# Performance work log

Measured on AMD Instinct MI355X. Metric: run time of the kernel, lower is better.

## Reference

```python
import jax, jax.numpy as jnp
import numpy as np

IN_DIM, OUT_DIM = 256, 10
N_EXPERTS, N_MEM, STEPS, N_SUB, MAX_K = 12, 32, 6, 5, 5
EXPERT_DIMS = [2048, 2560, 3072, 3584, 4096, 2304, 2816, 3328, 3840, 4608, 3072, 4096]
MAX_E = 4608
N_ITEMS = 4096
SCALE = IN_DIM ** -0.5

def _gelu(x):
    return jax.nn.gelu(x, approximate=False)

_ACTS = [jax.nn.silu, _gelu, lambda x: x * jnp.tanh(jax.nn.softplus(x)), jax.nn.relu,
         jax.nn.selu, jnp.tanh, jax.nn.softplus, jax.nn.elu]
EXPERT_ACTS = [_ACTS[i % 8] for i in range(N_EXPERTS)]

def _ln(x, s, b, eps=1e-5):
    mu = jnp.mean(x, -1, keepdims=True)
    var = jnp.mean((x - mu) ** 2, -1, keepdims=True)
    return (x - mu) * jax.lax.rsqrt(var + eps) * s + b

def _cell(x, ln_s, ln_b, w1, b1, w2, b2):
    h = _gelu(_ln(x, ln_s, ln_b) @ w1.T + b1)
    return x + h @ w2.T + b2

def _ctx_attn(cur, bank, qw, kw, vw):
    q = cur @ qw.T
    k = bank @ kw.T
    v = bank @ vw.T
    attn = jax.nn.softmax(jnp.einsum('nd,ntd->nt', q, k) * SCALE, axis=-1)
    return jnp.einsum('nt,ntd->nd', attn, v)

def _renorm_sparse_topk(probs, active_k):
    tv, ti = jax.lax.top_k(probs, MAX_K)
    mask = (jnp.arange(MAX_K)[None, :] < active_k[:, None]).astype(probs.dtype)
    vals = tv * mask
    rows = jnp.arange(probs.shape[0])[:, None]
    sparse = jnp.zeros_like(probs).at[rows, ti].set(vals)
    return sparse / jnp.maximum(jnp.sum(sparse, -1, keepdims=True), 1e-6)

def _fwd(x, W, b,
         shared_up_w, shared_down_w, shared_ln_s, shared_ln_b, shared_scale,
         mem_keys, mem_vals, mem_q_w, mem_out_w, mem_wg_w, mem_wg_b, mem_wv_w, mem_wv_b,
         depth_q_w, depth_k_w, depth_v_w, depth_out_w,
         rc_ln_s, rc_ln_b, rc_w1, rc_b1, rc_w2, rc_b2,
         ssm_in_w, ssm_out_w, ssm_decay,
         sub_w, sub_b, gate_w, gate_b,
         budget_w, budget_b,
         exp_up, exp_down, exp_ln_s, exp_ln_b,
         halt_w, halt_b,
         aux_up_w, aux_down_w, aux_ln_s, aux_ln_b, aux_gate_w, aux_gate_b,
         rf_ln_s, rf_ln_b, rf_w1, rf_b1, rf_w2, rf_b2, reflect_out_w,
         coll_q_w, coll_k_w, coll_v_w, coll_out_w,
         revisit_w, revisit_b,
         vc_ln_s, vc_ln_b, vc_w1, vc_b1, vc_w2, vc_b2,
         ver_q_w, ver_k_w, ver_v_w, ver_out_w, ver_gate_w, ver_gate_b, correction_out_w,
         mix):
    n = x.shape[0]
    base = x @ W.T + b
    shared = _ln(jax.nn.silu(x @ shared_up_w.T) @ shared_down_w.T, shared_ln_s, shared_ln_b)
    aux = _ln(_gelu(x @ aux_up_w.T) @ aux_down_w.T, aux_ln_s, aux_ln_b)

    mem_vals_b = jnp.broadcast_to(mem_vals[None], (n, N_MEM, IN_DIM))
    current = x
    mem_logits = jnp.zeros_like(base)
    depth_logits = jnp.zeros_like(base)
    cum_halt = jnp.zeros((n, 1), x.dtype)
    bank = []
    for s in range(STEPS):
        q = current @ mem_q_w.T
        attn = jax.nn.softmax((q @ mem_keys.T) * SCALE, axis=-1)
        mem_read = jnp.einsum('ns,nsd->nd', attn, mem_vals_b)
        wg = jax.nn.sigmoid(jnp.concatenate([current, mem_read], -1) @ mem_wg_w.T + mem_wg_b)
        wv = current @ mem_wv_w.T + mem_wv_b
        mem_vals_b = mem_vals_b * (1.0 - wg[..., None]) + wg[..., None] * wv[:, None, :]
        if bank:
            depth_ctx = _ctx_attn(current, jnp.stack(bank, 1), depth_q_w, depth_k_w, depth_v_w)
        else:
            depth_ctx = jnp.zeros_like(current)
        current = _cell(current + mem_read + depth_ctx,
                        rc_ln_s[s], rc_ln_b[s], rc_w1[s], rc_b1[s], rc_w2[s], rc_b2[s])
        h = jnp.tanh(current @ ssm_in_w.T) * jax.nn.sigmoid(ssm_decay)
        current = current + h @ ssm_out_w.T
        bank.append(current)
        halt = jax.nn.sigmoid((current @ halt_w[s])[:, None] + halt_b[s])
        w_step = (1.0 - cum_halt) * halt
        mem_logits = mem_logits + w_step * (mem_read @ mem_out_w.T)
        depth_logits = depth_logits + w_step * (depth_ctx @ depth_out_w.T)
        cum_halt = jnp.minimum(cum_halt + halt, 1.0)

    sub_logits = jnp.einsum('nd,sed->nse', current, sub_w) + sub_b
    sub_probs = jax.nn.softmax(sub_logits, axis=-1)
    gate = jax.nn.softmax(current @ gate_w.T + gate_b, axis=-1)
    probs = jnp.einsum('ns,nse->ne', gate, sub_probs)
    active_k = jnp.argmax(current @ budget_w.T + budget_b, axis=-1) + 1
    sparse = _renorm_sparse_topk(probs, active_k)

    expert_out = jnp.zeros_like(base)
    for i in range(N_EXPERTS):
        h = EXPERT_ACTS[i](current @ exp_up[i].T)
        o = _ln(h @ exp_down[i].T, exp_ln_s[i], exp_ln_b[i])
        expert_out = expert_out + sparse[:, i:i + 1] * o

    r = current
    for i in range(3):
        r = _cell(r, rf_ln_s[i], rf_ln_b[i], rf_w1[i], rf_b1[i], rf_w2[i], rf_b2[i])
    reflect_logits = r @ reflect_out_w.T

    stack = jnp.stack(bank, 1)
    coll_ctx = _ctx_attn(current, stack, coll_q_w, coll_k_w, coll_v_w)
    coll_logits = coll_ctx @ coll_out_w.T
    revisit = jax.nn.sigmoid(jnp.concatenate([x, current, coll_ctx], -1) @ revisit_w.T + revisit_b)

    v = current
    for i in range(2):
        v = _cell(v, vc_ln_s[i], vc_ln_b[i], vc_w1[i], vc_b1[i], vc_w2[i], vc_b2[i])
    ver_ctx = _ctx_attn(v, stack, ver_q_w, ver_k_w, ver_v_w)
    vg = jax.nn.softmax(jnp.concatenate([v, ver_ctx], -1) @ ver_gate_w.T + ver_gate_b, axis=-1)
    ver_logits = ver_ctx @ ver_out_w.T
    corr_logits = v @ correction_out_w.T

    ag = jax.nn.softmax(x @ aux_gate_w.T + aux_gate_b, axis=-1)
    alpha, beta, gamma, delta, eps_, zeta = [jnp.tanh(mix[i]) for i in range(6)]
    logits = (base
              + shared_scale * (ag[:, :1] * shared + ag[:, 1:] * aux)
              + alpha * expert_out
              + beta * mem_logits + zeta * depth_logits
              + gamma * reflect_logits
              + delta * revisit * coll_logits
              + eps_ * (vg[:, :1] * ver_logits + vg[:, 1:] * corr_logits))
    return logits


def setup_inputs() -> dict:
    key = jax.random.key(0)
    ks = iter(jax.random.split(key, 128))
    def nrm(shape, std=0.02):
        return jax.random.normal(next(ks), shape, jnp.float32) * std
    d, o = IN_DIM, OUT_DIM
    inp = dict(
        x=jax.random.normal(next(ks), (N_ITEMS, d), jnp.float32),
        W=nrm((o, d), 0.05), b=jnp.zeros((o,), jnp.float32),
        shared_up_w=nrm((3072, d)), shared_down_w=nrm((o, 3072)),
        shared_ln_s=jnp.ones((o,)), shared_ln_b=jnp.zeros((o,)),
        shared_scale=jnp.float32(1.0),
        mem_keys=nrm((N_MEM, d)), mem_vals=nrm((N_MEM, d)),
        mem_q_w=nrm((d, d), 0.01), mem_out_w=nrm((o, d), 0.01),
        mem_wg_w=nrm((N_MEM, 2 * d), 0.01), mem_wg_b=jnp.zeros((N_MEM,)),
        mem_wv_w=nrm((d, d), 0.01), mem_wv_b=jnp.zeros((d,)),
        depth_q_w=nrm((d, d), 0.01), depth_k_w=nrm((d, d), 0.01),
        depth_v_w=nrm((d, d), 0.01), depth_out_w=nrm((o, d), 0.01),
        rc_ln_s=jnp.ones((STEPS, d)), rc_ln_b=jnp.zeros((STEPS, d)),
        rc_w1=nrm((STEPS, 896, d)), rc_b1=jnp.zeros((STEPS, 896)),
        rc_w2=nrm((STEPS, d, 896)), rc_b2=jnp.zeros((STEPS, d)),
        ssm_in_w=nrm((48, d)), ssm_out_w=nrm((d, 48)), ssm_decay=jnp.zeros((48,)),
        sub_w=nrm((N_SUB, N_EXPERTS, d)), sub_b=jnp.zeros((N_SUB, N_EXPERTS)),
        gate_w=nrm((N_SUB, d)), gate_b=jnp.zeros((N_SUB,)),
        budget_w=nrm((MAX_K, d), 0.01), budget_b=jnp.zeros((MAX_K,)),
        halt_w=nrm((STEPS, d), 0.01), halt_b=jnp.full((STEPS,), -2.0, jnp.float32),
        aux_up_w=nrm((4096, d)), aux_down_w=nrm((o, 4096)),
        aux_ln_s=jnp.ones((o,)), aux_ln_b=jnp.zeros((o,)),
        aux_gate_w=nrm((2, d), 0.01), aux_gate_b=jnp.zeros((2,)),
        rf_ln_s=jnp.ones((3, d)), rf_ln_b=jnp.zeros((3, d)),
        rf_w1=nrm((3, 1280, d)), rf_b1=jnp.zeros((3, 1280)),
        rf_w2=nrm((3, d, 1280)), rf_b2=jnp.zeros((3, d)),
        reflect_out_w=nrm((o, d), 0.01),
        coll_q_w=nrm((d, d), 0.01), coll_k_w=nrm((d, d), 0.01),
        coll_v_w=nrm((d, d), 0.01), coll_out_w=nrm((o, d), 0.01),
        revisit_w=nrm((1, 3 * d), 0.01), revisit_b=jnp.zeros((1,)),
        vc_ln_s=jnp.ones((2, d)), vc_ln_b=jnp.zeros((2, d)),
        vc_w1=nrm((2, 1536, d)), vc_b1=jnp.zeros((2, 1536)),
        vc_w2=nrm((2, d, 1536)), vc_b2=jnp.zeros((2, d)),
        ver_q_w=nrm((d, d), 0.01), ver_k_w=nrm((d, d), 0.01),
        ver_v_w=nrm((d, d), 0.01), ver_out_w=nrm((o, d), 0.01),
        ver_gate_w=nrm((2, 2 * d), 0.01), ver_gate_b=jnp.zeros((2,)),
        correction_out_w=nrm((o, d), 0.01),
        mix=jnp.full((6,), 0.5, jnp.float32),
    )
    up = jax.random.normal(next(ks), (N_EXPERTS, MAX_E, d), jnp.float32) * 0.02
    down = jax.random.normal(next(ks), (N_EXPERTS, o, MAX_E), jnp.float32) * 0.01
    col = jnp.arange(MAX_E)
    dims = jnp.array(EXPERT_DIMS)
    mask = (col[None, :] < dims[:, None]).astype(jnp.float32)
    inp['exp_up'] = up * mask[:, :, None]
    inp['exp_down'] = down * mask[:, None, :]
    inp['exp_ln_s'] = jnp.ones((N_EXPERTS, o))
    inp['exp_ln_b'] = jnp.zeros((N_EXPERTS, o))
    return inp


def reference(x, W, b,
              shared_up_w, shared_down_w, shared_ln_s, shared_ln_b, shared_scale,
              mem_keys, mem_vals, mem_q_w, mem_out_w, mem_wg_w, mem_wg_b, mem_wv_w, mem_wv_b,
              depth_q_w, depth_k_w, depth_v_w, depth_out_w,
              rc_ln_s, rc_ln_b, rc_w1, rc_b1, rc_w2, rc_b2,
              ssm_in_w, ssm_out_w, ssm_decay,
              sub_w, sub_b, gate_w, gate_b,
              budget_w, budget_b,
              exp_up, exp_down, exp_ln_s, exp_ln_b,
              halt_w, halt_b,
              aux_up_w, aux_down_w, aux_ln_s, aux_ln_b, aux_gate_w, aux_gate_b,
              rf_ln_s, rf_ln_b, rf_w1, rf_b1, rf_w2, rf_b2, reflect_out_w,
              coll_q_w, coll_k_w, coll_v_w, coll_out_w,
              revisit_w, revisit_b,
              vc_ln_s, vc_ln_b, vc_w1, vc_b1, vc_w2, vc_b2,
              ver_q_w, ver_k_w, ver_v_w, ver_out_w, ver_gate_w, ver_gate_b, correction_out_w,
              mix):
    return _fwd(x, W, b,
                shared_up_w, shared_down_w, shared_ln_s, shared_ln_b, shared_scale,
                mem_keys, mem_vals, mem_q_w, mem_out_w, mem_wg_w, mem_wg_b, mem_wv_w, mem_wv_b,
                depth_q_w, depth_k_w, depth_v_w, depth_out_w,
                rc_ln_s, rc_ln_b, rc_w1, rc_b1, rc_w2, rc_b2,
                ssm_in_w, ssm_out_w, ssm_decay,
                sub_w, sub_b, gate_w, gate_b,
                budget_w, budget_b,
                exp_up, exp_down, exp_ln_s, exp_ln_b,
                halt_w, halt_b,
                aux_up_w, aux_down_w, aux_ln_s, aux_ln_b, aux_gate_w, aux_gate_b,
                rf_ln_s, rf_ln_b, rf_w1, rf_b1, rf_w2, rf_b2, reflect_out_w,
                coll_q_w, coll_k_w, coll_v_w, coll_out_w,
                revisit_w, revisit_b,
                vc_ln_s, vc_ln_b, vc_w1, vc_b1, vc_w2, vc_b2,
                ver_q_w, ver_k_w, ver_v_w, ver_out_w, ver_gate_w, ver_gate_b, correction_out_w,
                mix)
```

## Files before the change

### kernel.cpp

```cpp
#include <hip/hip_runtime.h>


constexpr int NI      = 4096;
constexpr int DIM     = 256;
constexpr int ODIM    = 10;
constexpr int NMEM_   = 32;
constexpr int NSTEPS_ = 6;
constexpr int NEXPERT_= 12;
constexpr int MAXE    = 4608;
constexpr int TOTCOL  = 46592;
#define SCL 0.0625f

__constant__ int GCNT[14]   = {8,10,12,14,16,9,11,13,15,18,12,16,12,16};
__constant__ int GSTART[14] = {0,8,18,30,44,60,69,80,93,108,126,138,154,166};
__constant__ int CCNT[14]   = {32,40,48,56,64,36,44,52,60,72,48,64,48,64};
__constant__ int ZCOL[14]   = {0,2048,4608,7680,11264,15360,17664,20480,
                               23808,27648,32256,35328,39424,42496};

typedef __attribute__((ext_vector_type(8))) short short8v;
typedef __attribute__((ext_vector_type(4))) float float4v;
typedef __attribute__((ext_vector_type(4))) unsigned short ushort4v;


__device__ __forceinline__ float wred_sum(float v){
  #pragma unroll
  for (int m = 32; m > 0; m >>= 1) v += __shfl_xor(v, m, 64);
  return v;
}
__device__ __forceinline__ float wred_max(float v){
  #pragma unroll
  for (int m = 32; m > 0; m >>= 1) v = fmaxf(v, __shfl_xor(v, m, 64));
  return v;
}
__device__ __forceinline__ float sigm(float x){ return 1.f/(1.f + __expf(-x)); }
__device__ __forceinline__ float tanh_f(float x){
  float e = __expf(2.f*fabsf(x));
  float r = 1.f - 2.f/(e + 1.f);
  return copysignf(r, x);
}
__device__ __forceinline__ float erf_f(float x){
  float ax = fabsf(x);
  float t = 1.f/fmaf(0.3275911f, ax, 1.f);
  float p = t*(0.254829592f + t*(-0.284496736f + t*(1.421413741f +
            t*(-1.453152027f + t*1.061405429f))));
  float r = 1.f - p*__expf(-ax*ax);
  return copysignf(r, x);
}
__device__ __forceinline__ float geluf(float x){
  return 0.5f*x*(1.f + erf_f(x*0.70710678118654752f));
}
__device__ __forceinline__ float softplusf(float x){
  return fmaxf(x, 0.f) + __logf(1.f + __expf(-fabsf(x)));
}
__device__ __forceinline__ float act_apply(int a, float x){
  switch(a){
    case 0: return x*sigm(x);
    case 1: return geluf(x);
    case 2: return x*tanh_f(softplusf(x));
    case 3: return fmaxf(x, 0.f);
    case 4: { const float l=1.0507009873554805f, al=1.6732632423543772f;
              return x > 0.f ? l*x : l*al*(__expf(x)-1.f); }
    case 5: return tanh_f(x);
    case 6: return softplusf(x);
    default: return x > 0.f ? x : __expf(x)-1.f;
  }
}
__device__ __forceinline__ unsigned short f2b(float f){
  unsigned u = __float_as_uint(f);
  u = u + 0x7FFFu + ((u >> 16) & 1u);
  return (unsigned short)(u >> 16);
}
__device__ __forceinline__ float b2f(unsigned short u){
  return __uint_as_float((unsigned)u << 16);
}
__device__ __forceinline__ float dot256f(const float* __restrict__ a,
                                         const float* __restrict__ w, float s){
  for (int k = 0; k < DIM; k += 4){
    float4 av = *(const float4*)&a[k];
    float4 wv = *(const float4*)&w[k];
    s = fmaf(av.x,wv.x, fmaf(av.y,wv.y, fmaf(av.z,wv.z, fmaf(av.w,wv.w, s))));
  }
  return s;
}
__device__ __forceinline__ void ln10(const float* p, const float* s, const float* b, float* o){
  float mu = 0.f;
  #pragma unroll
  for (int i=0;i<ODIM;i++) mu += p[i];
  mu *= 0.1f;
  float var = 0.f;
  #pragma unroll
  for (int i=0;i<ODIM;i++){ float d = p[i]-mu; var += d*d; }
  var *= 0.1f;
  float rs = 1.f/sqrtf(var + 1e-5f);
  #pragma unroll
  for (int i=0;i<ODIM;i++) o[i] = (p[i]-mu)*rs*s[i] + b[i];
}

__global__ __launch_bounds__(256)
void cvt_k(const float* __restrict__ in, unsigned short* __restrict__ out, int n)
{
  int idx = (blockIdx.x*256 + threadIdx.x)*4;
  if (idx + 3 < n){
    float4 v = *(const float4*)&in[idx];
    ushort4v t; t[0]=f2b(v.x); t[1]=f2b(v.y); t[2]=f2b(v.z); t[3]=f2b(v.w);
    *(ushort4v*)&out[idx] = t;
  }
}

__global__ __launch_bounds__(512)
void cvtup_k(const float* __restrict__ exp_up, const float* __restrict__ shared_up,
             const float* __restrict__ aux_up, short* __restrict__ upb)
{
  int chunk = blockIdx.x;
  int z = 0, crem = chunk;
  while (crem >= CCNT[z]){ crem -= CCNT[z]; z++; }
  const float* src;
  if (z < 12)       src = exp_up + (size_t)z*MAXE*DIM;
  else if (z == 12) src = shared_up;
  else              src = aux_up;
  int colbase = crem*64;
  short* dst = upb + (size_t)chunk*16384;
  int t = threadIdx.x;
  int c = t >> 3, kb = (t & 7)*32;
  const float* srow = src + (size_t)(colbase + c)*DIM + kb;
  #pragma unroll
  for (int j = 0; j < 4; j++){
    float4 f0 = *(const float4*)&srow[j*8];
    float4 f1 = *(const float4*)&srow[j*8+4];
    short8v s;
    s[0]=(short)f2b(f0.x); s[1]=(short)f2b(f0.y); s[2]=(short)f2b(f0.z); s[3]=(short)f2b(f0.w);
    s[4]=(short)f2b(f1.x); s[5]=(short)f2b(f1.y); s[6]=(short)f2b(f1.z); s[7]=(short)f2b(f1.w);
    int kq = (t & 7)*4 + j;
    *(short8v*)&dst[((size_t)kq*64 + c)*8] = s;
  }
}

template<int EPI>
__global__ __launch_bounds__(256)
void gemm_k(const float* __restrict__ A, const float* __restrict__ W,
            const float* __restrict__ bias, const float* __restrict__ R,
            float* __restrict__ C, float* __restrict__ C2, int N, int K)
{
  __shared__ float As[32][68];
  __shared__ float Ws[32][68];
  const int bm = blockIdx.y*64, bn = blockIdx.x*64;
  const int tid = threadIdx.x;
  const int tx = tid & 15, ty = tid >> 4;
  const int lrow = tid >> 2, lkq = (tid & 3) * 8;
  float acc[4][4] = {};
  for (int k0 = 0; k0 < K; k0 += 32){
    #pragma unroll
    for (int h = 0; h < 2; ++h){
      int kk = lkq + h*4;
      float4 va = *(const float4*)&A[(size_t)(bm+lrow)*K + k0 + kk];
      float4 vw = *(const float4*)&W[(size_t)(bn+lrow)*K + k0 + kk];
      As[kk+0][lrow]=va.x; As[kk+1][lrow]=va.y; As[kk+2][lrow]=va.z; As[kk+3][lrow]=va.w;
      Ws[kk+0][lrow]=vw.x; Ws[kk+1][lrow]=vw.y; Ws[kk+2][lrow]=vw.z; Ws[kk+3][lrow]=vw.w;
    }
    __syncthreads();
    #pragma unroll
    for (int kk = 0; kk < 32; ++kk){
      float4 a4 = *(const float4*)&As[kk][ty*4];
      float4 b4 = *(const float4*)&Ws[kk][tx*4];
      float av[4] = {a4.x,a4.y,a4.z,a4.w};
      float bv[4] = {b4.x,b4.y,b4.z,b4.w};
      #pragma unroll
      for (int i=0;i<4;i++)
        #pragma unroll
        for (int j=0;j<4;j++) acc[i][j] = fmaf(av[i], bv[j], acc[i][j]);
    }
    __syncthreads();
  }
  #pragma unroll
  for (int i=0;i<4;i++){
    int r = bm + ty*4 + i;
    #pragma unroll
    for (int j=0;j<4;j++){
      int c = bn + tx*4 + j;
      float v = acc[i][j];
      if constexpr (EPI==0){ C[(size_t)r*N + c] = v; }
      else if constexpr (EPI==1){ C[(size_t)r*N + c] = v + bias[c]; }
      else if constexpr (EPI==2){ C[(size_t)r*N + c] = geluf(v + bias[c]); }
      else if constexpr (EPI==3){ C[(size_t)r*N + c] = v + bias[c] + R[(size_t)r*N + c]; }
      else if constexpr (EPI==6){
        if (c < 256) C[(size_t)r*256 + c] = v + bias[c];
        else C2[(size_t)r*256 + (c-256)] = v;
      }
    }
  }
}

__global__ __launch_bounds__(256)
void gemm_rc1_k(const float* __restrict__ A, const float* __restrict__ W,
                const float* __restrict__ bias, float* __restrict__ C,
                int N, int K)
{
  __shared__ float As[32][132];
  __shared__ float Ws[32][68];
  const int bm = blockIdx.y*128, bn = blockIdx.x*64;
  const int tid = threadIdx.x;
  const int tx = tid & 15, ty = tid >> 4;
  const int arow = tid >> 1, ak = (tid & 1)*16;
  const int brow = tid >> 2, bk = (tid & 3)*8;
  float acc[8][4] = {};
  for (int k0 = 0; k0 < K; k0 += 32){
    float4 a0 = *(const float4*)&A[(size_t)(bm+arow)*K + k0 + ak];
    float4 a1 = *(const float4*)&A[(size_t)(bm+arow)*K + k0 + ak + 4];
    float4 a2 = *(const float4*)&A[(size_t)(bm+arow)*K + k0 + ak + 8];
    float4 a3 = *(const float4*)&A[(size_t)(bm+arow)*K + k0 + ak + 12];
    float4 b0 = *(const float4*)&W[(size_t)(bn+brow)*K + k0 + bk];
    float4 b1 = *(const float4*)&W[(size_t)(bn+brow)*K + k0 + bk + 4];
    As[ak+ 0][arow]=a0.x; As[ak+ 1][arow]=a0.y; As[ak+ 2][arow]=a0.z; As[ak+ 3][arow]=a0.w;
    As[ak+ 4][arow]=a1.x; As[ak+ 5][arow]=a1.y; As[ak+ 6][arow]=a1.z; As[ak+ 7][arow]=a1.w;
    As[ak+ 8][arow]=a2.x; As[ak+ 9][arow]=a2.y; As[ak+10][arow]=a2.z; As[ak+11][arow]=a2.w;
    As[ak+12][arow]=a3.x; As[ak+13][arow]=a3.y; As[ak+14][arow]=a3.z; As[ak+15][arow]=a3.w;
    Ws[bk+0][brow]=b0.x; Ws[bk+1][brow]=b0.y; Ws[bk+2][brow]=b0.z; Ws[bk+3][brow]=b0.w;
    Ws[bk+4][brow]=b1.x; Ws[bk+5][brow]=b1.y; Ws[bk+6][brow]=b1.z; Ws[bk+7][brow]=b1.w;
    __syncthreads();
    #pragma unroll
    for (int kk = 0; kk < 32; ++kk){
      float a8[8];
      *(float4*)&a8[0] = *(const float4*)&As[kk][ty*8];
      *(float4*)&a8[4] = *(const float4*)&As[kk][ty*8+4];
      float4 b4 = *(const float4*)&Ws[kk][tx*4];
      float bv[4] = {b4.x,b4.y,b4.z,b4.w};
      #pragma unroll
      for (int i=0;i<8;i++)
        #pragma unroll
        for (int j=0;j<4;j++) acc[i][j] = fmaf(a8[i], bv[j], acc[i][j]);
    }
    __syncthreads();
  }
  #pragma unroll
  for (int i=0;i<8;i++){
    int r = bm + ty*8 + i;
    #pragma unroll
    for (int j=0;j<4;j++){
      int c = bn + tx*4 + j;
      C[(size_t)r*N + c] = geluf(acc[i][j] + bias[c]);
    }
  }
}

template<int EPI>
__global__ __launch_bounds__(256)
void bgemm_k(const short* __restrict__ A, const short* __restrict__ B,
             const float* __restrict__ bias, const float* __restrict__ R,
             float* __restrict__ Cf, unsigned short* __restrict__ Cb,
             int N, int K)
{
  __shared__ short As[128][40];
  __shared__ short Bsm[64][40];
  const int bm = blockIdx.y*128, bn = blockIdx.x*64;
  const int tid = threadIdx.x;
  const int wave = tid >> 6, lane = tid & 63;
  const int l15 = lane & 15, lg = lane >> 4;
  const int ar = tid >> 1, ah = tid & 1;
  float4v acc[2][4] = {};
  for (int k0 = 0; k0 < K; k0 += 32){
    __syncthreads();
    { const short* src = A + (size_t)(bm+ar)*K + k0 + ah*16;
      short8v v0 = *(const short8v*)src;
      short8v v1 = *(const short8v*)(src+8);
      *(short8v*)&As[ar][ah*16]   = v0;
      *(short8v*)&As[ar][ah*16+8] = v1; }
    if (tid < 128){
      const short* src = B + (size_t)(bn+ar)*K + k0 + ah*16;
      short8v v0 = *(const short8v*)src;
      short8v v1 = *(const short8v*)(src+8);
      *(short8v*)&Bsm[ar][ah*16]   = v0;
      *(short8v*)&Bsm[ar][ah*16+8] = v1; }
    __syncthreads();
    short8v bfr[4];
    #pragma unroll
    for (int nt = 0; nt < 4; nt++)
      bfr[nt] = *(const short8v*)&Bsm[nt*16 + l15][lg*8];
    #pragma unroll
    for (int mt = 0; mt < 2; mt++){
      short8v a = *(const short8v*)&As[wave*32 + mt*16 + l15][lg*8];
      #pragma unroll
      for (int nt = 0; nt < 4; nt++)
        acc[mt][nt] = __builtin_amdgcn_mfma_f32_16x16x32_bf16(a, bfr[nt], acc[mt][nt], 0, 0, 0);
    }
  }
  #pragma unroll
  for (int mt = 0; mt < 2; mt++)
    #pragma unroll
    for (int nt = 0; nt < 4; nt++)
      #pragma unroll
      for (int reg = 0; reg < 4; reg++){
        int row = bm + wave*32 + mt*16 + lg*4 + reg;
        int col = bn + nt*16 + l15;
        float v = acc[mt][nt][reg];
        if constexpr (EPI==0){
          v = geluf(v + bias[col]);
          Cb[(size_t)row*N + col] = f2b(v);
        } else {
          v = v + bias[col] + R[(size_t)row*N + col];
          Cf[(size_t)row*N + col] = v;
        }
      }
}

template<int ACT>
__global__ __launch_bounds__(512)
void moe6_k(const unsigned short* __restrict__ curb, const unsigned short* __restrict__ xb,
            const short* __restrict__ upb,
            const float* __restrict__ exp_down, const float* __restrict__ shared_down,
            const float* __restrict__ aux_down,
            const int* __restrict__ idxl, const int* __restrict__ cnt,
            unsigned short* __restrict__ part,
            int z0, int z1, int z2)
{
  __shared__ short Bs[16384];
  __shared__ float Ds[64][12];
  int gy = blockIdx.y;
  int z = z0;
  if (z1 >= 0 && gy >= GCNT[z]){
    gy -= GCNT[z]; z = z1;
    if (z2 >= 0 && gy >= GCNT[z]){ gy -= GCNT[z]; z = z2; }
  }
  const int n = (z < 12) ? cnt[z] : NI;
  const int bm = blockIdx.x*128;
  if (bm >= n) return;
  const int g = GSTART[z] + gy;
  const int localcol = gy*256;
  int dstride; const float* down;
  if (z < 12){ down = exp_down + (size_t)z*ODIM*MAXE; dstride = MAXE; }
  else if (z == 12){ down = shared_down; dstride = 3072; }
  else { down = aux_down; dstride = 4096; }
  const unsigned short* X = (z < 12) ? curb : xb;
  const int tid = threadIdx.x, wave = tid >> 6, lane = tid & 63;
  const int l15 = lane & 15, lg = lane >> 4;

  int slotA = bm + wave*16 + l15;
  int itemA;
  if (z < 12) itemA = idxl[(size_t)z*NI + ((slotA < n) ? slotA : (n-1))];
  else        itemA = slotA;

  short8v afrag[8];
  { const unsigned short* xr = X + (size_t)itemA*DIM;
    #pragma unroll
    for (int ks = 0; ks < 8; ks++)
      afrag[ks] = *(const short8v*)&xr[ks*32 + lg*8];
  }
  float racc[4][10];
  #pragma unroll
  for (int r = 0; r < 4; r++)
    #pragma unroll
    for (int o = 0; o < 10; o++) racc[r][o] = 0.f;

  const int gchunk0 = (ZCOL[z] + localcol) >> 6;
  const int dso = tid >> 6, dse = tid & 63;

  short8v p0, p1, p2, p3;
  float e0, e1;
  auto ldchunk = [&](int ch){
    const short* chunk = upb + ((size_t)(gchunk0 + ch))*16384;
    p0 = *(const short8v*)&chunk[(size_t)(tid       )*8];
    p1 = *(const short8v*)&chunk[(size_t)(tid +  512)*8];
    p2 = *(const short8v*)&chunk[(size_t)(tid + 1024)*8];
    p3 = *(const short8v*)&chunk[(size_t)(tid + 1536)*8];
    int cb = localcol + ch*64;
    e0 = down[(size_t)dso*dstride + cb + dse];
    e1 = (tid < 128) ? down[(size_t)(dso+8)*dstride + cb + dse] : 0.f;
  };
  auto stu = [&](int u, short8v v){
    int c = u & 63, kq = u >> 6;
    int byteoff = ((c << 9) + (kq << 4)) ^ ((c & 7) << 4);
    *(short8v*)((char*)Bs + byteoff) = v;
  };

  ldchunk(0);
  for (int ch = 0; ch < 4; ++ch){
    stu(tid, p0); stu(tid + 512, p1); stu(tid + 1024, p2); stu(tid + 1536, p3);
    Ds[dse][dso] = e0;
    if (tid < 128) Ds[dse][dso + 8] = e1;
    __syncthreads();
    if (ch < 3) ldchunk(ch + 1);
    float4v acc[4] = {};
    #pragma unroll
    for (int ks = 0; ks < 8; ks++)
      #pragma unroll
      for (int nt = 0; nt < 4; nt++){
        int c = nt*16 + l15, kq = ks*4 + lg;
        int byteoff = ((c << 9) + (kq << 4)) ^ ((c & 7) << 4);
        short8v b = *(const short8v*)((const char*)Bs + byteoff);
        acc[nt] = __builtin_amdgcn_mfma_f32_16x16x32_bf16(afrag[ks], b, acc[nt], 0, 0, 0);
      }
    #pragma unroll
    for (int nt = 0; nt < 4; nt++){
      const float* dp = &Ds[nt*16 + l15][0];
      float4 dv0 = *(const float4*)dp;
      float4 dv1 = *(const float4*)(dp + 4);
      float  d8 = dp[8], d9 = dp[9];
      float dv[10] = {dv0.x,dv0.y,dv0.z,dv0.w,dv1.x,dv1.y,dv1.z,dv1.w,d8,d9};
      float hv[4];
      #pragma unroll
      for (int reg = 0; reg < 4; reg++) hv[reg] = act_apply(ACT, acc[nt][reg]);
      #pragma unroll
      for (int o = 0; o < 10; o++)
        #pragma unroll
        for (int reg = 0; reg < 4; reg++)
          racc[reg][o] = fmaf(hv[reg], dv[o], racc[reg][o]);
    }
    __syncthreads();
  }
  #pragma unroll
  for (int reg = 0; reg < 4; reg++)
    #pragma unroll
    for (int o = 0; o < 10; o++){
      float v = racc[reg][o];
      v += __shfl_xor(v, 1, 64); v += __shfl_xor(v, 2, 64);
      v += __shfl_xor(v, 4, 64); v += __shfl_xor(v, 8, 64);
      racc[reg][o] = v;
    }
  if (l15 == 0){
    #pragma unroll
    for (int reg = 0; reg < 4; reg++){
      int slotW = bm + wave*16 + lg*4 + reg;
      int itemW;
      if (z < 12) itemW = idxl[(size_t)z*NI + ((slotW < n) ? slotW : (n-1))];
      else        itemW = slotW;
      #pragma unroll
      for (int o = 0; o < 10; o++)
        part[((size_t)g*NI + itemW)*ODIM + o] = f2b(racc[reg][o]);
    }
  }
}

__global__ __launch_bounds__(256)
void red_k(const unsigned short* __restrict__ part, float* __restrict__ expert_pre,
           float* __restrict__ shared_pre, float* __restrict__ aux_pre)
{
  int idx = blockIdx.x*256 + threadIdx.x;
  if (idx >= 14*NI*ODIM) return;
  int z = idx / (NI*ODIM), rem = idx - z*NI*ODIM;
  float s = 0.f;
  int g0 = GSTART[z], gn = GCNT[z];
  for (int g2 = 0; g2 < gn; g2++)
    s += b2f(part[(size_t)(g0 + g2)*NI*ODIM + rem]);
  if (z < 12) expert_pre[(size_t)z*NI*ODIM + rem] = s;
  else if (z == 12) shared_pre[rem] = s;
  else aux_pre[rem] = s;
}

__global__ void atb_k(const float* __restrict__ A, const float* __restrict__ B,
                      float* __restrict__ C, int M, int I, int J)
{
  int idx = blockIdx.x*256 + threadIdx.x;
  if (idx >= I*J) return;
  int i = idx / J, j = idx - i*J;
  float s = 0.f;
  for (int m = 0; m < M; m++) s = fmaf(A[(size_t)m*I+i], B[(size_t)m*J+j], s);
  C[idx] = s;
}
__global__ void ab_k(const float* __restrict__ A, const float* __restrict__ B,
                     float* __restrict__ C, int M, int K, int N)
{
  int idx = blockIdx.x*256 + threadIdx.x;
  if (idx >= M*N) return;
  int i = idx / N, j = idx - i*N;
  float s = 0.f;
  for (int k = 0; k < K; k++) s = fmaf(A[(size_t)i*K+k], B[(size_t)k*N+j], s);
  C[idx] = s;
}

__global__ __launch_bounds__(256)
void ln3_k(const float* __restrict__ a, const float* __restrict__ b,
           const float* __restrict__ c, const float* __restrict__ lns,
           const float* __restrict__ lnb, float* __restrict__ xout,
           float* __restrict__ lnout, unsigned short* __restrict__ lnout_b)
{
  int item = blockIdx.x*4 + (threadIdx.x >> 6);
  int lane = threadIdx.x & 63;
  float4 v = ((const float4*)(a + (size_t)item*DIM))[lane];
  if (b){ float4 t = ((const float4*)(b + (size_t)item*DIM))[lane]; v.x+=t.x; v.y+=t.y; v.z+=t.z; v.w+=t.w; }
  if (c){ float4 t = ((const float4*)(c + (size_t)item*DIM))[lane]; v.x+=t.x; v.y+=t.y; v.z+=t.z; v.w+=t.w; }
  if (xout) ((float4*)(xout + (size_t)item*DIM))[lane] = v;
  float mu = wred_sum(v.x+v.y+v.z+v.w) * (1.f/DIM);
  float dx=v.x-mu, dy=v.y-mu, dz=v.z-mu, dw=v.w-mu;
  float var = wred_sum(dx*dx+dy*dy+dz*dz+dw*dw) * (1.f/DIM);
  float rs = 1.f/sqrtf(var + 1e-5f);
  float4 s4 = ((const float4*)lns)[lane];
  float4 b4 = ((const float4*)lnb)[lane];
  float4 o4 = make_float4(dx*rs*s4.x + b4.x, dy*rs*s4.y + b4.y,
                          dz*rs*s4.z + b4.z, dw*rs*s4.w + b4.w);
  if (lnout) ((float4*)(lnout + (size_t)item*DIM))[lane] = o4;
  if (lnout_b){
    ushort4v t; t[0]=f2b(o4.x); t[1]=f2b(o4.y); t[2]=f2b(o4.z); t[3]=f2b(o4.w);
    *(ushort4v*)(lnout_b + (size_t)item*DIM + lane*4) = t;
  }
}

__global__ __launch_bounds__(256)
void memrw_k(const float* __restrict__ cur, const float* __restrict__ MK,
             const float* __restrict__ mem_vals, const float* __restrict__ wv_hist,
             const float* __restrict__ mem_wg_w, const float* __restrict__ mem_wg_b,
             float* __restrict__ a_state, float* __restrict__ c_state,
             float* __restrict__ mem_read, int step)
{
  __shared__ float smem[4][DIM];
  int wi = threadIdx.x >> 6;
  int item = blockIdx.x*4 + wi;
  int lane = threadIdx.x & 63;
  float v = -1e30f;
  if (lane < NMEM_)
    v = dot256f(cur + (size_t)item*DIM, MK + (size_t)lane*DIM, 0.f) * SCL;
  float m = wred_max(v);
// ... 422 lines not shown
  const float* vc_b1         = (const float*)d_in[59];
  const float* vc_w2         = (const float*)d_in[60];
  const float* vc_b2         = (const float*)d_in[61];
  const float* ver_q_w       = (const float*)d_in[62];
  const float* ver_k_w       = (const float*)d_in[63];
  const float* ver_v_w       = (const float*)d_in[64];
  const float* ver_out_w     = (const float*)d_in[65];
  const float* ver_gate_w    = (const float*)d_in[66];
  const float* ver_gate_b    = (const float*)d_in[67];
  const float* correction_out_w = (const float*)d_in[68];
  const float* mix           = (const float*)d_in[69];
  const float* exp_up        = (const float*)d_in[70];
  const float* exp_down      = (const float*)d_in[71];
  const float* exp_ln_s      = (const float*)d_in[72];
  const float* exp_ln_b      = (const float*)d_in[73];
  float* out = (float*)d_out;

  float* w = (float*)d_ws;
  size_t off = 0;
  auto WS = [&](size_t nf){ float* p = w + off; off += nf; return p; };
  float* bank      = WS((size_t)NSTEPS_*NI*DIM);
  float* rbuf      = WS((size_t)NI*DIM);
  float* vbuf      = WS((size_t)NI*DIM);
  float* coll_ctx  = WS((size_t)NI*DIM);
  float* ver_ctx   = WS((size_t)NI*DIM);
  float* q2        = WS((size_t)NI*DIM);
  float* wsumb     = WS((size_t)NI*DIM);
  float* sparse    = WS((size_t)NI*NEXPERT_);
  float* base10    = WS((size_t)NI*ODIM);
  float* reflect10 = WS((size_t)NI*ODIM);
  float* coll10    = WS((size_t)NI*ODIM);
  float* ver10     = WS((size_t)NI*ODIM);
  float* corr10    = WS((size_t)NI*ODIM);
  float* PcT       = WS((size_t)DIM*DIM);
  float* PvT       = WS((size_t)DIM*DIM);
  float* MK        = WS((size_t)NMEM_*DIM);
  float* Wvq       = WS((size_t)512*DIM);
  float* expert_pre= WS((size_t)NEXPERT_*NI*ODIM);
  float* shared_pre= WS((size_t)NI*ODIM);
  float* aux_pre   = WS((size_t)NI*ODIM);
  unsigned short* cur_b = (unsigned short*)WS((size_t)NI*DIM/2);
  unsigned short* x_b   = (unsigned short*)WS((size_t)NI*DIM/2);
  int* idxl        = (int*)WS((size_t)NEXPERT_*NI);
  float* S72       = WS((size_t)NI*72);
  int* cnt         = (int*)WS(16);
  float* zbase     = w + off;
  float* mem_logits   = WS((size_t)NI*ODIM);
  float* depth_logits = WS((size_t)NI*ODIM);
  float* cum_halt     = WS((size_t)NI);
  size_t zbytes = (size_t)((w + off) - zbase) * sizeof(float);
  hipMemsetAsync((void*)zbase, 0, zbytes, stream);

  float* U = w + off;
  float* wv_hist   = U;
  float* hbig      = U + (size_t)NSTEPS_*NI*DIM;
  float* cur_in    = hbig + (size_t)NI*896;
  float* t_ln      = cur_in + (size_t)NI*DIM;
  float* mem_read  = t_ln + (size_t)NI*DIM;
  float* depth_ctx = mem_read + (size_t)NI*DIM;
  float* a_state   = depth_ctx + (size_t)NI*DIM;
  float* c_state   = a_state + (size_t)NI*NMEM_;
  unsigned short* upb    = (unsigned short*)U;
  unsigned short* hb     = (unsigned short*)U;
  float* ovl = U + 5963776;
  unsigned short* t_ln_b = (unsigned short*)ovl;          ovl += 524288;
  unsigned short* rfw1b  = (unsigned short*)ovl;          ovl += 491520;
  unsigned short* rfw2b  = (unsigned short*)ovl;          ovl += 491520;
  unsigned short* vcw1b  = (unsigned short*)ovl;          ovl += 393216;
  unsigned short* vcw2b  = (unsigned short*)ovl;          ovl += 393216;
  unsigned short* part   = (unsigned short*)ovl;

  hipMemcpyAsync(Wvq, mem_wv_w, (size_t)DIM*DIM*sizeof(float),
                 hipMemcpyDeviceToDevice, stream);
  atb_k<<<(DIM*DIM+255)/256, 256, 0, stream>>>(depth_k_w, depth_q_w, Wvq + (size_t)DIM*DIM, DIM, DIM, DIM);
  atb_k<<<(DIM*DIM+255)/256, 256, 0, stream>>>(coll_k_w,  coll_q_w,  PcT, DIM, DIM, DIM);
  atb_k<<<(DIM*DIM+255)/256, 256, 0, stream>>>(ver_k_w,   ver_q_w,   PvT, DIM, DIM, DIM);
  ab_k <<<(NMEM_*DIM+255)/256, 256, 0, stream>>>(mem_keys, mem_q_w, MK, NMEM_, DIM, DIM);

  const float* cur = x;
  for (int s = 0; s < NSTEPS_; s++){
    memrw_k<<<NI/4, 256, 0, stream>>>(cur, MK, mem_vals, wv_hist,
                                      mem_wg_w, mem_wg_b, a_state, c_state,
                                      mem_read, s);
    gemm_k<6><<<dim3(8, NI/64), 256, 0, stream>>>(
        cur, Wvq, mem_wv_b, nullptr, wv_hist + (size_t)s*NI*DIM, q2, 512, DIM);
    if (s > 0){
      bankattn_k<<<NI/4, 256, 0, stream>>>(q2, bank, wsumb, s);
      gemm_k<0><<<dim3(4, NI/64), 256, 0, stream>>>(
          wsumb, depth_v_w, nullptr, nullptr, depth_ctx, nullptr, DIM, DIM);
    }
    ln3_k<<<NI/4, 256, 0, stream>>>(cur, mem_read, (s > 0 ? depth_ctx : nullptr),
                                    rc_ln_s + (size_t)s*DIM, rc_ln_b + (size_t)s*DIM,
                                    cur_in, t_ln, nullptr);
    gemm_rc1_k<<<dim3(14, NI/128), 256, 0, stream>>>(
        t_ln, rc_w1 + (size_t)s*896*DIM, rc_b1 + (size_t)s*896, hbig, 896, DIM);
    gemm_k<3><<<dim3(4, NI/64), 256, 0, stream>>>(
        hbig, rc_w2 + (size_t)s*DIM*896, rc_b2 + (size_t)s*DIM, cur_in,
        cur_in, nullptr, DIM, 896);
    float* newcur = bank + (size_t)s*NI*DIM;
    ssmhalt_k<<<NI/4, 256, 0, stream>>>(cur_in, mem_read, depth_ctx,
                                        ssm_in_w, ssm_out_w, ssm_decay,
                                        halt_w, halt_b, mem_out_w, depth_out_w,
                                        newcur, mem_logits, depth_logits, cum_halt, s);
    cur = newcur;
  }

  thin70_k<<<(NI*70 + 255)/256, 256, 0, stream>>>(
      cur, sub_w, sub_b, gate_w, gate_b, budget_w, budget_b, S72);
  topk_k<<<(NI + 255)/256, 256, 0, stream>>>(S72, sparse);
  buildlist_k<<<NEXPERT_, 256, 0, stream>>>(sparse, idxl, cnt);

  launch_cvt(cur, cur_b, (size_t)NI*DIM, stream);
  launch_cvt(x,   x_b,   (size_t)NI*DIM, stream);
  cvtup_k<<<TOTCOL/64, 512, 0, stream>>>(exp_up, shared_up_w, aux_up_w, (short*)upb);
  launch_cvt(rf_w1, rfw1b, (size_t)3*1280*DIM, stream);
  launch_cvt(rf_w2, rfw2b, (size_t)3*DIM*1280, stream);
  launch_cvt(vc_w1, vcw1b, (size_t)2*1536*DIM, stream);
  launch_cvt(vc_w2, vcw2b, (size_t)2*DIM*1536, stream);

  {
    #define MOE_LAUNCH(ACT, NG, Z0, Z1, Z2)                                   \
      moe6_k<ACT><<<dim3(NI/128, NG), 512, 0, stream>>>(                      \
          cur_b, x_b, (const short*)upb, exp_down, shared_down_w, aux_down_w, \
          idxl, cnt, part, Z0, Z1, Z2)
    MOE_LAUNCH(1, 44, 1, 9, 13);
    MOE_LAUNCH(0, 35, 0, 8, 12);
    MOE_LAUNCH(3, 30, 3, 11, -1);
    MOE_LAUNCH(2, 24, 2, 10, -1);
    MOE_LAUNCH(4, 16, 4, -1, -1);
    MOE_LAUNCH(7, 13, 7, -1, -1);
    MOE_LAUNCH(6, 11, 6, -1, -1);
    MOE_LAUNCH(5,  9, 5, -1, -1);
    #undef MOE_LAUNCH
  }
  red_k<<<(14*NI*ODIM + 255)/256, 256, 0, stream>>>(part, expert_pre, shared_pre, aux_pre);

  const float* rsrc = cur;
  for (int i = 0; i < 3; i++){
    ln3_k<<<NI/4, 256, 0, stream>>>(rsrc, nullptr, nullptr,
                                    rf_ln_s + (size_t)i*DIM, rf_ln_b + (size_t)i*DIM,
                                    nullptr, nullptr, t_ln_b);
    bgemm_k<0><<<dim3(1280/64, NI/128), 256, 0, stream>>>(
        (const short*)t_ln_b, (const short*)(rfw1b + (size_t)i*1280*DIM),
        rf_b1 + (size_t)i*1280, nullptr, nullptr, hb, 1280, DIM);
    bgemm_k<1><<<dim3(DIM/64, NI/128), 256, 0, stream>>>(
        (const short*)hb, (const short*)(rfw2b + (size_t)i*DIM*1280),
        rf_b2 + (size_t)i*DIM, rsrc, rbuf, nullptr, DIM, 1280);
    rsrc = rbuf;
  }

  const float* vsrc = cur;
  for (int i = 0; i < 2; i++){
    ln3_k<<<NI/4, 256, 0, stream>>>(vsrc, nullptr, nullptr,
                                    vc_ln_s + (size_t)i*DIM, vc_ln_b + (size_t)i*DIM,
                                    nullptr, nullptr, t_ln_b);
    bgemm_k<0><<<dim3(1536/64, NI/128), 256, 0, stream>>>(
        (const short*)t_ln_b, (const short*)(vcw1b + (size_t)i*1536*DIM),
        vc_b1 + (size_t)i*1536, nullptr, nullptr, hb, 1536, DIM);
    bgemm_k<1><<<dim3(DIM/64, NI/128), 256, 0, stream>>>(
        (const short*)hb, (const short*)(vcw2b + (size_t)i*DIM*1536),
        vc_b2 + (size_t)i*DIM, vsrc, vbuf, nullptr, DIM, 1536);
    vsrc = vbuf;
  }

  gemm_k<0><<<dim3(4, NI/64), 256, 0, stream>>>(
      cur, PcT, nullptr, nullptr, q2, nullptr, DIM, DIM);
  bankattn_k<<<NI/4, 256, 0, stream>>>(q2, bank, wsumb, NSTEPS_);
  gemm_k<0><<<dim3(4, NI/64), 256, 0, stream>>>(
      wsumb, coll_v_w, nullptr, nullptr, coll_ctx, nullptr, DIM, DIM);

  gemm_k<0><<<dim3(4, NI/64), 256, 0, stream>>>(
      vbuf, PvT, nullptr, nullptr, q2, nullptr, DIM, DIM);
  bankattn_k<<<NI/4, 256, 0, stream>>>(q2, bank, wsumb, NSTEPS_);
  gemm_k<0><<<dim3(4, NI/64), 256, 0, stream>>>(
      wsumb, ver_v_w, nullptr, nullptr, ver_ctx, nullptr, DIM, DIM);

  heads_k<<<(NI*50 + 255)/256, 256, 0, stream>>>(
      rbuf, coll_ctx, ver_ctx, vbuf, x,
      reflect_out_w, coll_out_w, ver_out_w, correction_out_w, Wm, bvec,
      reflect10, coll10, ver10, corr10, base10);

  final_k<<<(NI+255)/256, 256, 0, stream>>>(
      x, cur, vbuf, coll_ctx, ver_ctx,
      base10, shared_pre, aux_pre, expert_pre, sparse,
      mem_logits, depth_logits, reflect10, coll10, ver10, corr10,
      shared_ln_s, shared_ln_b, aux_ln_s, aux_ln_b, exp_ln_s, exp_ln_b,
      aux_gate_w, aux_gate_b, ver_gate_w, ver_gate_b, revisit_w, revisit_b,
      shared_scale, mix, out);
}
```

Before: 2.820 ms.

## Fuse residual LayerNorm into rc1 GEMM, merge MoE launches, skip unused projections

```diff
diff --git a/kernel.cpp b/kernel.cpp
--- a/kernel.cpp
+++ b/kernel.cpp
@@ -51,19 +51,6 @@
 }
 __device__ __forceinline__ float softplusf(float x){
   return fmaxf(x, 0.f) + __logf(1.f + __expf(-fabsf(x)));
-}
-__device__ __forceinline__ float act_apply(int a, float x){
-  switch(a){
-    case 0: return x*sigm(x);
-    case 1: return geluf(x);
-    case 2: return x*tanh_f(softplusf(x));
-    case 3: return fmaxf(x, 0.f);
-    case 4: { const float l=1.0507009873554805f, al=1.6732632423543772f;
-              return x > 0.f ? l*x : l*al*(__expf(x)-1.f); }
-    case 5: return tanh_f(x);
-    case 6: return softplusf(x);
-    default: return x > 0.f ? x : __expf(x)-1.f;
-  }
 }
 __device__ __forceinline__ unsigned short f2b(float f){
   unsigned u = __float_as_uint(f);
@@ -180,7 +167,6 @@
       float v = acc[i][j];
       if constexpr (EPI==0){ C[(size_t)r*N + c] = v; }
       else if constexpr (EPI==1){ C[(size_t)r*N + c] = v + bias[c]; }
-      else if constexpr (EPI==2){ C[(size_t)r*N + c] = geluf(v + bias[c]); }
       else if constexpr (EPI==3){ C[(size_t)r*N + c] = v + bias[c] + R[(size_t)r*N + c]; }
       else if constexpr (EPI==6){
         if (c < 256) C[(size_t)r*256 + c] = v + bias[c];
@@ -191,32 +177,66 @@
 }
 
 __global__ __launch_bounds__(256)
-void gemm_rc1_k(const float* __restrict__ A, const float* __restrict__ W,
-                const float* __restrict__ bias, float* __restrict__ C,
-                int N, int K)
+void gemm_rc1ln_k(const float* __restrict__ cur, const float* __restrict__ memr,
+                  const float* __restrict__ depth,
+                  const float* __restrict__ lns, const float* __restrict__ lnb,
+                  const float* __restrict__ W, const float* __restrict__ bias,
+                  float* __restrict__ cur_in, float* __restrict__ C, int N)
 {
   __shared__ float As[32][132];
   __shared__ float Ws[32][68];
+  __shared__ float MU[128], RS[128];
   const int bm = blockIdx.y*128, bn = blockIdx.x*64;
   const int tid = threadIdx.x;
-  const int tx = tid & 15, ty = tid >> 4;
+  const int wave = tid >> 6, lane = tid & 63;
+  for (int rr = wave; rr < 128; rr += 4){
+    int row = bm + rr;
+    float4 v = ((const float4*)(cur + (size_t)row*DIM))[lane];
+    { float4 t = ((const float4*)(memr + (size_t)row*DIM))[lane];
+      v.x+=t.x; v.y+=t.y; v.z+=t.z; v.w+=t.w; }
+    if (depth){ float4 t = ((const float4*)(depth + (size_t)row*DIM))[lane];
+      v.x+=t.x; v.y+=t.y; v.z+=t.z; v.w+=t.w; }
+    if (blockIdx.x == 0)
+      ((float4*)(cur_in + (size_t)row*DIM))[lane] = v;
+    float mu = wred_sum(v.x+v.y+v.z+v.w) * (1.f/DIM);
+    float dx=v.x-mu, dy=v.y-mu, dz=v.z-mu, dw=v.w-mu;
+    float var = wred_sum(dx*dx+dy*dy+dz*dz+dw*dw) * (1.f/DIM);
+    float rs = 1.f/sqrtf(var + 1e-5f);
+    if (lane == 0){ MU[rr] = mu; RS[rr] = rs; }
+  }
+  __syncthreads();
   const int arow = tid >> 1, ak = (tid & 1)*16;
   const int brow = tid >> 2, bk = (tid & 3)*8;
+  const float mu = MU[arow], rs = RS[arow];
   float acc[8][4] = {};
-  for (int k0 = 0; k0 < K; k0 += 32){
-    float4 a0 = *(const float4*)&A[(size_t)(bm+arow)*K + k0 + ak];
-    float4 a1 = *(const float4*)&A[(size_t)(bm+arow)*K + k0 + ak + 4];
-    float4 a2 = *(const float4*)&A[(size_t)(bm+arow)*K + k0 + ak + 8];
-    float4 a3 = *(const float4*)&A[(size_t)(bm+arow)*K + k0 + ak + 12];
-    float4 b0 = *(const float4*)&W[(size_t)(bn+brow)*K + k0 + bk];
-    float4 b1 = *(const float4*)&W[(size_t)(bn+brow)*K + k0 + bk + 4];
-    As[ak+ 0][arow]=a0.x; As[ak+ 1][arow]=a0.y; As[ak+ 2][arow]=a0.z; As[ak+ 3][arow]=a0.w;
-    As[ak+ 4][arow]=a1.x; As[ak+ 5][arow]=a1.y; As[ak+ 6][arow]=a1.z; As[ak+ 7][arow]=a1.w;
-    As[ak+ 8][arow]=a2.x; As[ak+ 9][arow]=a2.y; As[ak+10][arow]=a2.z; As[ak+11][arow]=a2.w;
-    As[ak+12][arow]=a3.x; As[ak+13][arow]=a3.y; As[ak+14][arow]=a3.z; As[ak+15][arow]=a3.w;
+  for (int k0 = 0; k0 < DIM; k0 += 32){
+    float4 a[4], lsv[4], lbv[4];
+    #pragma unroll
+    for (int i=0;i<4;i++){
+      int kk = k0 + ak + 4*i;
+      float4 v = *(const float4*)&cur[(size_t)(bm+arow)*DIM + kk];
+      float4 t = *(const float4*)&memr[(size_t)(bm+arow)*DIM + kk];
+      v.x+=t.x; v.y+=t.y; v.z+=t.z; v.w+=t.w;
+      if (depth){ t = *(const float4*)&depth[(size_t)(bm+arow)*DIM + kk];
+        v.x+=t.x; v.y+=t.y; v.z+=t.z; v.w+=t.w; }
+      a[i] = v;
+      lsv[i] = *(const float4*)&lns[kk];
+      lbv[i] = *(const float4*)&lnb[kk];
+    }
+    float4 b0 = *(const float4*)&W[(size_t)(bn+brow)*DIM + k0 + bk];
+    float4 b1 = *(const float4*)&W[(size_t)(bn+brow)*DIM + k0 + bk + 4];
+    #pragma unroll
+    for (int i=0;i<4;i++){
+      float dx=a[i].x-mu, dy=a[i].y-mu, dz=a[i].z-mu, dw=a[i].w-mu;
+      As[ak+4*i+0][arow] = dx*rs*lsv[i].x + lbv[i].x;
+      As[ak+4*i+1][arow] = dy*rs*lsv[i].y + lbv[i].y;
+      As[ak+4*i+2][arow] = dz*rs*lsv[i].z + lbv[i].z;
+      As[ak+4*i+3][arow] = dw*rs*lsv[i].w + lbv[i].w;
+    }
     Ws[bk+0][brow]=b0.x; Ws[bk+1][brow]=b0.y; Ws[bk+2][brow]=b0.z; Ws[bk+3][brow]=b0.w;
     Ws[bk+4][brow]=b1.x; Ws[bk+5][brow]=b1.y; Ws[bk+6][brow]=b1.z; Ws[bk+7][brow]=b1.w;
     __syncthreads();
+    const int tx = tid & 15, ty = tid >> 4;
     #pragma unroll
     for (int kk = 0; kk < 32; ++kk){
       float a8[8];
@@ -231,6 +251,7 @@
     }
     __syncthreads();
   }
+  const int tx = tid & 15, ty = tid >> 4;
   #pragma unroll
   for (int i=0;i<8;i++){
     int r = bm + ty*8 + i;
@@ -302,33 +323,27 @@
       }
 }
 
-template<int ACT>
 __global__ __launch_bounds__(512)
-void moe6_k(const unsigned short* __restrict__ curb, const unsigned short* __restrict__ xb,
+void moe7_k(const unsigned short* __restrict__ curb, const unsigned short* __restrict__ xb,
             const short* __restrict__ upb,
             const float* __restrict__ exp_down, const float* __restrict__ shared_down,
             const float* __restrict__ aux_down,
             const int* __restrict__ idxl, const int* __restrict__ cnt,
-            unsigned short* __restrict__ part,
-            int z0, int z1, int z2)
+            unsigned short* __restrict__ part)
 {
   __shared__ short Bs[16384];
   __shared__ float Ds[64][12];
-  int gy = blockIdx.y;
-  int z = z0;
-  if (z1 >= 0 && gy >= GCNT[z]){
-    gy -= GCNT[z]; z = z1;
-    if (z2 >= 0 && gy >= GCNT[z]){ gy -= GCNT[z]; z = z2; }
-  }
+  int gy = blockIdx.y, z = 0;
+  while (gy >= GCNT[z]){ gy -= GCNT[z]; z++; }
   const int n = (z < 12) ? cnt[z] : NI;
   const int bm = blockIdx.x*128;
   if (bm >= n) return;
   const int g = GSTART[z] + gy;
   const int localcol = gy*256;
-  int dstride; const float* down;
-  if (z < 12){ down = exp_down + (size_t)z*ODIM*MAXE; dstride = MAXE; }
-  else if (z == 12){ down = shared_down; dstride = 3072; }
-  else { down = aux_down; dstride = 4096; }
+  int act, dstride; const float* down;
+  if (z < 12){ act = z & 7; down = exp_down + (size_t)z*ODIM*MAXE; dstride = MAXE; }
+  else if (z == 12){ act = 0; down = shared_down; dstride = 3072; }
+  else { act = 1; down = aux_down; dstride = 4096; }
   const unsigned short* X = (z < 12) ? curb : xb;
   const int tid = threadIdx.x, wave = tid >> 6, lane = tid & 63;
   const int l15 = lane & 15, lg = lane >> 4;
@@ -388,6 +403,61 @@
         short8v b = *(const short8v*)((const char*)Bs + byteoff);
         acc[nt] = __builtin_amdgcn_mfma_f32_16x16x32_bf16(afrag[ks], b, acc[nt], 0, 0, 0);
       }
+    float hv[4][4];
+    switch(act){
+      case 0:
+        #pragma unroll
+        for (int nt=0;nt<4;nt++)
+          #pragma unroll
+          for (int r=0;r<4;r++){ float xx=acc[nt][r]; hv[nt][r]=xx*sigm(xx); }
+        break;
+      case 1:
+        #pragma unroll
+        for (int nt=0;nt<4;nt++)
+          #pragma unroll
+          for (int r=0;r<4;r++){ hv[nt][r]=geluf(acc[nt][r]); }
+        break;
+      case 2:
+        #pragma unroll
+        for (int nt=0;nt<4;nt++)
+          #pragma unroll
+          for (int r=0;r<4;r++){ float xx=acc[nt][r]; hv[nt][r]=xx*tanh_f(softplusf(xx)); }
+        break;
+      case 3:
+        #pragma unroll
+        for (int nt=0;nt<4;nt++)
+          #pragma unroll
+          for (int r=0;r<4;r++){ hv[nt][r]=fmaxf(acc[nt][r],0.f); }
+        break;
+      case 4:
+        #pragma unroll
+        for (int nt=0;nt<4;nt++)
+          #pragma unroll
+          for (int r=0;r<4;r++){
+            const float l=1.0507009873554805f, al=1.6732632423543772f;
+            float xx=acc[nt][r];
+            hv[nt][r] = xx>0.f ? l*xx : l*al*(__expf(xx)-1.f);
+          }
+        break;
+      case 5:
+        #pragma unroll
+        for (int nt=0;nt<4;nt++)
+          #pragma unroll
+          for (int r=0;r<4;r++){ hv[nt][r]=tanh_f(acc[nt][r]); }
+        break;
+      case 6:
+        #pragma unroll
+        for (int nt=0;nt<4;nt++)
+          #pragma unroll
+          for (int r=0;r<4;r++){ hv[nt][r]=softplusf(acc[nt][r]); }
+        break;
+      default:
+        #pragma unroll
+        for (int nt=0;nt<4;nt++)
+          #pragma unroll
+          for (int r=0;r<4;r++){ float xx=acc[nt][r]; hv[nt][r]= xx>0.f ? xx : __expf(xx)-1.f; }
+        break;
+    }
     #pragma unroll
     for (int nt = 0; nt < 4; nt++){
       const float* dp = &Ds[nt*16 + l15][0];
@@ -395,36 +465,33 @@
       float4 dv1 = *(const float4*)(dp + 4);
       float  d8 = dp[8], d9 = dp[9];
       float dv[10] = {dv0.x,dv0.y,dv0.z,dv0.w,dv1.x,dv1.y,dv1.z,dv1.w,d8,d9};
-      float hv[4];
-      #pragma unroll
-      for (int reg = 0; reg < 4; reg++) hv[reg] = act_apply(ACT, acc[nt][reg]);
       #pragma unroll
       for (int o = 0; o < 10; o++)
         #pragma unroll
-        for (int reg = 0; reg < 4; reg++)
-          racc[reg][o] = fmaf(hv[reg], dv[o], racc[reg][o]);
+        for (int r = 0; r < 4; r++)
+          racc[r][o] = fmaf(hv[nt][r], dv[o], racc[r][o]);
     }
     __syncthreads();
   }
   #pragma unroll
-  for (int reg = 0; reg < 4; reg++)
+  for (int r = 0; r < 4; r++)
     #pragma unroll
     for (int o = 0; o < 10; o++){
-      float v = racc[reg][o];
+      float v = racc[r][o];
       v += __shfl_xor(v, 1, 64); v += __shfl_xor(v, 2, 64);
       v += __shfl_xor(v, 4, 64); v += __shfl_xor(v, 8, 64);
-      racc[reg][o] = v;
+      racc[r][o] = v;
     }
   if (l15 == 0){
     #pragma unroll
-    for (int reg = 0; reg < 4; reg++){
-      int slotW = bm + wave*16 + lg*4 + reg;
+    for (int r = 0; r < 4; r++){
+      int slotW = bm + wave*16 + lg*4 + r;
       int itemW;
       if (z < 12) itemW = idxl[(size_t)z*NI + ((slotW < n) ? slotW : (n-1))];
       else        itemW = slotW;
       #pragma unroll
       for (int o = 0; o < 10; o++)
-        part[((size_t)g*NI + itemW)*ODIM + o] = f2b(racc[reg][o]);
+        part[((size_t)g*NI + itemW)*ODIM + o] = f2b(racc[r][o]);
     }
   }
 }
@@ -1013,18 +1080,26 @@
     memrw_k<<<NI/4, 256, 0, stream>>>(cur, MK, mem_vals, wv_hist,
                                       mem_wg_w, mem_wg_b, a_state, c_state,
                                       mem_read, s);
-    gemm_k<6><<<dim3(8, NI/64), 256, 0, stream>>>(
-        cur, Wvq, mem_wv_b, nullptr, wv_hist + (size_t)s*NI*DIM, q2, 512, DIM);
+    if (s == 0){
+      gemm_k<1><<<dim3(4, NI/64), 256, 0, stream>>>(
+          cur, Wvq, mem_wv_b, nullptr, wv_hist, nullptr, DIM, DIM);
+    } else if (s == NSTEPS_-1){
+      gemm_k<0><<<dim3(4, NI/64), 256, 0, stream>>>(
+          cur, Wvq + (size_t)DIM*DIM, nullptr, nullptr, q2, nullptr, DIM, DIM);
+    } else {
+      gemm_k<6><<<dim3(8, NI/64), 256, 0, stream>>>(
+          cur, Wvq, mem_wv_b, nullptr, wv_hist + (size_t)s*NI*DIM, q2, 512, DIM);
+    }
     if (s > 0){
       bankattn_k<<<NI/4, 256, 0, stream>>>(q2, bank, wsumb, s);
       gemm_k<0><<<dim3(4, NI/64), 256, 0, stream>>>(
           wsumb, depth_v_w, nullptr, nullptr, depth_ctx, nullptr, DIM, DIM);
     }
-    ln3_k<<<NI/4, 256, 0, stream>>>(cur, mem_read, (s > 0 ? depth_ctx : nullptr),
-                                    rc_ln_s + (size_t)s*DIM, rc_ln_b + (size_t)s*DIM,
-                                    cur_in, t_ln, nullptr);
-    gemm_rc1_k<<<dim3(14, NI/128), 256, 0, stream>>>(
-        t_ln, rc_w1 + (size_t)s*896*DIM, rc_b1 + (size_t)s*896, hbig, 896, DIM);
+    gemm_rc1ln_k<<<dim3(14, NI/128), 256, 0, stream>>>(
+        cur, mem_read, (s > 0 ? depth_ctx : nullptr),
+        rc_ln_s + (size_t)s*DIM, rc_ln_b + (size_t)s*DIM,
+        rc_w1 + (size_t)s*896*DIM, rc_b1 + (size_t)s*896,
+        cur_in, hbig, 896);
     gemm_k<3><<<dim3(4, NI/64), 256, 0, stream>>>(
         hbig, rc_w2 + (size_t)s*DIM*896, rc_b2 + (size_t)s*DIM, cur_in,
         cur_in, nullptr, DIM, 896);
@@ -1049,21 +1124,9 @@
   launch_cvt(vc_w1, vcw1b, (size_t)2*1536*DIM, stream);
   launch_cvt(vc_w2, vcw2b, (size_t)2*DIM*1536, stream);
 
-  {
-    #define MOE_LAUNCH(ACT, NG, Z0, Z1, Z2)                                   \
-      moe6_k<ACT><<<dim3(NI/128, NG), 512, 0, stream>>>(                      \
-          cur_b, x_b, (const short*)upb, exp_down, shared_down_w, aux_down_w, \
-          idxl, cnt, part, Z0, Z1, Z2)
-    MOE_LAUNCH(1, 44, 1, 9, 13);
-    MOE_LAUNCH(0, 35, 0, 8, 12);
-    MOE_LAUNCH(3, 30, 3, 11, -1);
-    MOE_LAUNCH(2, 24, 2, 10, -1);
-    MOE_LAUNCH(4, 16, 4, -1, -1);
-    MOE_LAUNCH(7, 13, 7, -1, -1);
-    MOE_LAUNCH(6, 11, 6, -1, -1);
-    MOE_LAUNCH(5,  9, 5, -1, -1);
-    #undef MOE_LAUNCH
-  }
+  moe7_k<<<dim3(NI/128, 182), 512, 0, stream>>>(
+      cur_b, x_b, (const short*)upb, exp_down, shared_down_w, aux_down_w,
+      idxl, cnt, part);
   red_k<<<(14*NI*ODIM + 255)/256, 256, 0, stream>>>(part, expert_pre, shared_pre, aux_pre);
 
   const float* rsrc = cur;
```

New measurement: 3.075 ms. 9.0% more time.
